# Kernel optimization log

Measured on AMD Instinct MI355X. Metric: run time of the kernel, lower is better.

## Reference

```python
import jax, jax.numpy as jnp
import numpy as np

N = 100_000       # nodes
DEG = 16          # avg degree (fixed here)
E = N * DEG       # edges
IN_F, HID, OUT_F = 64, 32, 16
K, DIM = 3, 2     # n_kernels, pseudo-coordinate dim


def setup_inputs() -> dict:
    key = jax.random.key(0)
    k1, k2, k3, k4, k5, k6, k7 = jax.random.split(key, 7)
    row_ptr = jnp.arange(N + 1, dtype=jnp.int64) * DEG          # CSR offsets, fixed degree
    col_idx = jax.random.randint(k1, (E,), 0, N, dtype=jnp.int64)
    input_feature = jax.random.normal(k2, (N, IN_F), dtype=jnp.float32)
    p = jax.random.uniform(k3, (E, DIM), dtype=jnp.float32)      # pseudo-coordinates per edge
    mu = jax.random.normal(k4, (K, DIM), dtype=jnp.float32)
    sigma = jax.random.uniform(k5, (K, DIM), dtype=jnp.float32, minval=0.5, maxval=1.5)
    W1 = jax.random.normal(k6, (K, IN_F, HID), dtype=jnp.float32) * (1.0 / np.sqrt(IN_F))
    W2 = jax.random.normal(k7, (K, HID, OUT_F), dtype=jnp.float32) * (1.0 / np.sqrt(HID))
    return {"row_ptr": row_ptr, "col_idx": col_idx, "input_feature": input_feature,
            "p": p, "mu": mu, "sigma": sigma, "W1": W1, "W2": W2}


def _edge_gaussians(p, mu, sigma):
    # w[e,k] = exp(-0.5 * sum_d ((p[e,d]-mu[k,d])/sigma[k,d])^2)   [E,K]
    diff = p[:, None, :] - mu[None, :, :]                 # [E,K,D]
    inv_var = 1.0 / (sigma * sigma)                       # [K,D]
    return jnp.exp(-0.5 * jnp.sum(diff * diff * inv_var[None], axis=-1))


def _gmm_conv(row_ptr, col_idx, dst, x, gauss, W):
    # per-kernel linear transform first (dense GEMM), then irregular gather+scatter
    xW = jnp.einsum('nf,kfh->nkh', x, W)                  # [N,K,H]
    msg = jnp.einsum('ek,ekh->eh', gauss, xW[col_idx])    # gather + mix kernels  [E,H]
    n_nodes = row_ptr.shape[0] - 1
    return jax.ops.segment_sum(msg, dst, num_segments=n_nodes)  # scatter-add to dst rows


def reference(row_ptr, col_idx, input_feature, p, mu, sigma, W1, W2):
    n_nodes = row_ptr.shape[0] - 1
    deg = jnp.diff(row_ptr)
    dst = jnp.repeat(jnp.arange(n_nodes), deg, total_repeat_length=col_idx.shape[0])
    gauss = _edge_gaussians(p, mu, sigma)                 # shared by both layers
    h = _gmm_conv(row_ptr, col_idx, dst, input_feature, gauss, W1)
    out = _gmm_conv(row_ptr, col_idx, dst, h, gauss, W2)
    return out
```

## Files before the change

### kernel.cpp

```cpp
#include <hip/hip_runtime.h>
#include <hip/hip_fp16.h>


#define KK 3

using half8  = __attribute__((ext_vector_type(8))) _Float16;
using float4v = __attribute__((ext_vector_type(4))) float;

__global__ void prep_kernel(const float* __restrict__ p, const float* __restrict__ mu,
                            const float* __restrict__ sigma, float2* __restrict__ gaussh,
                            const float* __restrict__ x, __half* __restrict__ xh,
                            int E, int NX8) {
    int i = blockIdx.x * blockDim.x + threadIdx.x;
    if (i < E) {
        float p0 = p[2 * i], p1 = p[2 * i + 1];
        float g[KK];
#pragma unroll
        for (int k = 0; k < KK; ++k) {
            float m0 = mu[2 * k], m1 = mu[2 * k + 1];
            float s0 = sigma[2 * k], s1 = sigma[2 * k + 1];
            float d0 = p0 - m0, d1 = p1 - m1;
            float q = (d0 * d0) / (s0 * s0) + (d1 * d1) / (s1 * s1);
            g[k] = __expf(-0.5f * q);
        }
        union { __half h[4]; float2 v; } o;
        o.h[0] = __float2half(g[0]); o.h[1] = __float2half(g[1]);
        o.h[2] = __float2half(g[2]); o.h[3] = __float2half(0.f);
        gaussh[i] = o.v;
    }
    if (i < NX8) {
        float4 v0 = ((const float4*)x)[2 * i];
        float4 v1 = ((const float4*)x)[2 * i + 1];
        union { __half h[8]; float4 v; } o;
        o.h[0] = __float2half(v0.x); o.h[1] = __float2half(v0.y);
        o.h[2] = __float2half(v0.z); o.h[3] = __float2half(v0.w);
        o.h[4] = __float2half(v1.x); o.h[5] = __float2half(v1.y);
        o.h[6] = __float2half(v1.z); o.h[7] = __float2half(v1.w);
        ((float4*)xh)[i] = o.v;
    }
}

__global__ void pack_w(const float* __restrict__ W1, const float* __restrict__ W2,
                       __half* __restrict__ B1, __half* __restrict__ B2) {
    int t = blockIdx.x * blockDim.x + threadIdx.x;
    if (t < 6144) {
        int j = t & 7, lane = (t >> 3) & 63, grp = t >> 9;
        int ot = grp / 6, kb = grp % 6;
        int kidx = kb * 32 + (lane >> 4) * 8 + j;
        int o = ot * 16 + (lane & 15);
        B1[t] = __float2half(W1[kidx * 32 + o]);
    } else if (t < 6144 + 1536) {
        int t2 = t - 6144;
        int j = t2 & 7, lane = (t2 >> 3) & 63, kb = t2 >> 9;
        int kidx = kb * 32 + (lane >> 4) * 8 + j;
        int o = lane & 15;
        B2[t2] = __float2half(W2[kidx * 16 + o]);
    }
}

__device__ __forceinline__ void unpack8(float4 raw, float* f) {
    union { float4 v; __half2 h2[4]; } u;
    u.v = raw;
#pragma unroll
    for (int q = 0; q < 4; ++q) {
        float2 t = __half22float2(u.h2[q]);
        f[2 * q] = t.x; f[2 * q + 1] = t.y;
    }
}

template <int F>
__global__ __launch_bounds__(256) void gather_s(
    const int* __restrict__ row_ptr, const int* __restrict__ col_idx,
    const float2* __restrict__ gaussh, const __half* __restrict__ xh,
    __half* __restrict__ s, int N) {
    constexpr int TPN = F / 8;
    constexpr int J   = KK * F;

    const int t  = blockIdx.x * 256 + threadIdx.x;
    const int n  = t / TPN;
    const int ch = t % TPN;
    if (n >= N) return;

    float a0[8], a1[8], a2[8];
#pragma unroll
    for (int q = 0; q < 8; ++q) { a0[q] = 0.f; a1[q] = 0.f; a2[q] = 0.f; }

    const float4* x4 = (const float4*)xh;

    int e0 = row_ptr[n], e1 = row_ptr[n + 1];
    int e = e0;
    for (; e + 8 <= e1; e += 8) {
        int cols[8];
        float2 gr[8];
        float4 xr[8];
#pragma unroll
        for (int j = 0; j < 8; ++j) cols[j] = col_idx[e + j];
#pragma unroll
        for (int j = 0; j < 8; ++j) gr[j] = gaussh[e + j];
#pragma unroll
        for (int j = 0; j < 8; ++j) xr[j] = x4[(size_t)cols[j] * TPN + ch];
#pragma unroll
        for (int j = 0; j < 8; ++j) {
            union { float2 v; __half2 h2[2]; } ug; ug.v = gr[j];
            float2 gab = __half22float2(ug.h2[0]);
            float2 gc_ = __half22float2(ug.h2[1]);
            float f[8];
            unpack8(xr[j], f);
#pragma unroll
            for (int q = 0; q < 8; ++q) {
                a0[q] = fmaf(gab.x, f[q], a0[q]);
                a1[q] = fmaf(gab.y, f[q], a1[q]);
                a2[q] = fmaf(gc_.x, f[q], a2[q]);
            }
        }
    }
    for (; e < e1; ++e) {
        int c = col_idx[e];
        union { float2 v; __half2 h2[2]; } ug; ug.v = gaussh[e];
        float2 gab = __half22float2(ug.h2[0]);
        float2 gc_ = __half22float2(ug.h2[1]);
        float f[8];
        unpack8(x4[(size_t)c * TPN + ch], f);
#pragma unroll
        for (int q = 0; q < 8; ++q) {
            a0[q] = fmaf(gab.x, f[q], a0[q]);
            a1[q] = fmaf(gab.y, f[q], a1[q]);
            a2[q] = fmaf(gc_.x, f[q], a2[q]);
        }
    }

    __half* srow = s + (size_t)n * J + ch * 8;
    union { __half h[8]; float4 v; } o;
#pragma unroll
    for (int q = 0; q < 8; ++q) o.h[q] = __float2half(a0[q]);
    *(float4*)(srow + 0 * F) = o.v;
#pragma unroll
    for (int q = 0; q < 8; ++q) o.h[q] = __float2half(a1[q]);
    *(float4*)(srow + 1 * F) = o.v;
#pragma unroll
    for (int q = 0; q < 8; ++q) o.h[q] = __float2half(a2[q]);
    *(float4*)(srow + 2 * F) = o.v;
}

template <int J, int H, bool OUT_HALF>
__global__ __launch_bounds__(256) void gemm_mfma(
    const __half* __restrict__ s, const __half* __restrict__ Bpack,
    void* __restrict__ yout, int N) {
    constexpr int KB = J / 32;
    constexpr int OT = H / 16;

    const int lane = threadIdx.x & 63;
    const int gw   = (blockIdx.x * 256 + threadIdx.x) >> 6;
    const int nt   = gw / OT;
    const int ot   = gw % OT;
    const int n0   = nt * 16;
    if (n0 >= N) return;

    const int quad = lane >> 4;
    const int row  = lane & 15;

    half8 b[KB];
#pragma unroll
    for (int kb = 0; kb < KB; ++kb)
        b[kb] = ((const half8*)Bpack)[(ot * KB + kb) * 64 + lane];

    const half8* arow = (const half8*)(s + (size_t)(n0 + row) * J);

    float4v acc = {0.f, 0.f, 0.f, 0.f};
#pragma unroll
    for (int kb = 0; kb < KB; ++kb)
        acc = __builtin_amdgcn_mfma_f32_16x16x32_f16(arow[kb * 4 + quad], b[kb], acc, 0, 0, 0);

    const int col = row;
    const int r0  = quad * 4;
#pragma unroll
    for (int reg = 0; reg < 4; ++reg) {
        int n = n0 + r0 + reg;
        if constexpr (OUT_HALF)
            ((__half*)yout)[(size_t)n * H + ot * 16 + col] = __float2half(acc[reg]);
        else
            ((float*)yout)[(size_t)n * H + col] = acc[reg];
    }
}

extern "C" void kernel_launch(void* const* d_in, const int* in_sizes, int n_in,
                              void* d_out, int out_size, void* d_ws, size_t ws_size,
                              hipStream_t stream) {
    const int* row_ptr  = (const int*)d_in[0];
    const int* col_idx  = (const int*)d_in[1];
    const float* x      = (const float*)d_in[2];
    const float* p      = (const float*)d_in[3];
    const float* mu     = (const float*)d_in[4];
    const float* sigma  = (const float*)d_in[5];
    const float* W1     = (const float*)d_in[6];
    const float* W2     = (const float*)d_in[7];

    const int N = in_sizes[0] - 1;
    const int E = in_sizes[1];

    __half* B1pack = (__half*)d_ws;
    __half* B2pack = B1pack + 6144;
    float2* gaussh = (float2*)(B2pack + 1536);
    __half* xh     = (__half*)(gaussh + (size_t)E);
    __half* hh     = xh + (size_t)N * 64;
    __half* s1     = hh + (size_t)N * 32;
    __half* s2     = s1 + (size_t)N * 192;
    float*  out    = (float*)d_out;

    const int B = 256;
    const int NX8 = N * 8;
    const int prep_n = (E > NX8 ? E : NX8);

    prep_kernel<<<(prep_n + B - 1) / B, B, 0, stream>>>(p, mu, sigma, gaussh, x, xh, E, NX8);
    pack_w<<<30, B, 0, stream>>>(W1, W2, B1pack, B2pack);

    {
        long long T = (long long)N * 8;
        gather_s<64><<<(int)((T + B - 1) / B), B, 0, stream>>>(row_ptr, col_idx, gaussh, xh, s1, N);
        int waves = ((N + 15) / 16) * 2;
        gemm_mfma<192, 32, true><<<(waves + 3) / 4, B, 0, stream>>>(s1, B1pack, (void*)hh, N);
    }
    {
        long long T = (long long)N * 4;
        gather_s<32><<<(int)((T + B - 1) / B), B, 0, stream>>>(row_ptr, col_idx, gaussh, hh, s2, N);
        int waves = (N + 15) / 16;
        gemm_mfma<96, 16, false><<<(waves + 3) / 4, B, 0, stream>>>(s2, B2pack, (void*)out, N);
    }
}
```

Before: 179.5 us.

## Fuse gather and MFMA GEMM per layer via LDS, recompute Gaussians inline

Each layer's gather-aggregate and its MFMA GEMM now run in one kernel. The aggregated [nodes, 3F] tile is staged in padded shared memory instead of being written to and re-read from the global s1/s2 buffers. Edge Gaussian weights are recomputed from p inside both layers instead of being precomputed into a half buffer. Weight packing is merged into the x conversion kernel, cutting the launch count from six to three. In exchange, each layer reads 8 bytes of fp32 p per edge instead of the 8-byte half gauss record and evaluates three exps per edge per thread, repeated across the channel threads. The kernels also add LDS use and a block barrier.

Result: faster. 156.8 us (-12.6%).

```diff
diff --git a/kernel.cpp b/kernel.cpp
--- a/kernel.cpp
+++ b/kernel.cpp
@@ -4,57 +4,33 @@
 
 #define KK 3
 
-using half8  = __attribute__((ext_vector_type(8))) _Float16;
+using half8   = __attribute__((ext_vector_type(8))) _Float16;
 using float4v = __attribute__((ext_vector_type(4))) float;
 
-__global__ void prep_kernel(const float* __restrict__ p, const float* __restrict__ mu,
-                            const float* __restrict__ sigma, float2* __restrict__ gaussh,
-                            const float* __restrict__ x, __half* __restrict__ xh,
-                            int E, int NX8) {
-    int i = blockIdx.x * blockDim.x + threadIdx.x;
-    if (i < E) {
-        float p0 = p[2 * i], p1 = p[2 * i + 1];
-        float g[KK];
-#pragma unroll
-        for (int k = 0; k < KK; ++k) {
-            float m0 = mu[2 * k], m1 = mu[2 * k + 1];
-            float s0 = sigma[2 * k], s1 = sigma[2 * k + 1];
-            float d0 = p0 - m0, d1 = p1 - m1;
-            float q = (d0 * d0) / (s0 * s0) + (d1 * d1) / (s1 * s1);
-            g[k] = __expf(-0.5f * q);
-        }
-        union { __half h[4]; float2 v; } o;
-        o.h[0] = __float2half(g[0]); o.h[1] = __float2half(g[1]);
-        o.h[2] = __float2half(g[2]); o.h[3] = __float2half(0.f);
-        gaussh[i] = o.v;
-    }
-    if (i < NX8) {
-        float4 v0 = ((const float4*)x)[2 * i];
-        float4 v1 = ((const float4*)x)[2 * i + 1];
+__global__ void setup_kernel(const float* __restrict__ x, __half* __restrict__ xh,
+                             const float* __restrict__ W1, const float* __restrict__ W2,
+                             __half* __restrict__ B1, __half* __restrict__ B2, int NX8) {
+    int t = blockIdx.x * blockDim.x + threadIdx.x;
+    if (t < NX8) {
+        float4 v0 = ((const float4*)x)[2 * t];
+        float4 v1 = ((const float4*)x)[2 * t + 1];
         union { __half h[8]; float4 v; } o;
         o.h[0] = __float2half(v0.x); o.h[1] = __float2half(v0.y);
         o.h[2] = __float2half(v0.z); o.h[3] = __float2half(v0.w);
         o.h[4] = __float2half(v1.x); o.h[5] = __float2half(v1.y);
         o.h[6] = __float2half(v1.z); o.h[7] = __float2half(v1.w);
-        ((float4*)xh)[i] = o.v;
-    }
-}
-
-__global__ void pack_w(const float* __restrict__ W1, const float* __restrict__ W2,
-                       __half* __restrict__ B1, __half* __restrict__ B2) {
-    int t = blockIdx.x * blockDim.x + threadIdx.x;
+        ((float4*)xh)[t] = o.v;
+    }
     if (t < 6144) {
         int j = t & 7, lane = (t >> 3) & 63, grp = t >> 9;
         int ot = grp / 6, kb = grp % 6;
         int kidx = kb * 32 + (lane >> 4) * 8 + j;
-        int o = ot * 16 + (lane & 15);
-        B1[t] = __float2half(W1[kidx * 32 + o]);
+        B1[t] = __float2half(W1[kidx * 32 + ot * 16 + (lane & 15)]);
     } else if (t < 6144 + 1536) {
         int t2 = t - 6144;
         int j = t2 & 7, lane = (t2 >> 3) & 63, kb = t2 >> 9;
         int kidx = kb * 32 + (lane >> 4) * 8 + j;
-        int o = lane & 15;
-        B2[t2] = __float2half(W2[kidx * 16 + o]);
+        B2[t2] = __float2half(W2[kidx * 16 + (lane & 15)]);
     }
 }
 
@@ -68,118 +44,139 @@
     }
 }
 
-template <int F>
-__global__ __launch_bounds__(256) void gather_s(
+template <int F, int H, bool OUT_HALF>
+__global__ __launch_bounds__(256) void fused_layer(
     const int* __restrict__ row_ptr, const int* __restrict__ col_idx,
-    const float2* __restrict__ gaussh, const __half* __restrict__ xh,
-    __half* __restrict__ s, int N) {
-    constexpr int TPN = F / 8;
-    constexpr int J   = KK * F;
-
-    const int t  = blockIdx.x * 256 + threadIdx.x;
-    const int n  = t / TPN;
-    const int ch = t % TPN;
-    if (n >= N) return;
+    const float* __restrict__ p, const float* __restrict__ mu, const float* __restrict__ sigma,
+    const __half* __restrict__ xh, const __half* __restrict__ Bpack,
+    void* __restrict__ yout, int N) {
+    constexpr int TPN    = F / 8;
+    constexpr int NODES  = 256 / TPN;
+    constexpr int J      = KK * F;
+    constexpr int STRIDE = (F == 64) ? 200 : 104;
+    constexpr int KB     = J / 32;
+    constexpr int OT     = H / 16;
+    constexpr int TILES  = NODES / 16;
+
+    __shared__ __align__(16) __half sLh[NODES * STRIDE];
+
+    const int tid = threadIdx.x;
+    const int nl  = tid / TPN;
+    const int ch  = tid % TPN;
+    const int n   = blockIdx.x * NODES + nl;
+
+    float gm0[KK], gm1[KK], iv0[KK], iv1[KK];
+#pragma unroll
+    for (int k = 0; k < KK; ++k) {
+        gm0[k] = mu[2 * k];     gm1[k] = mu[2 * k + 1];
+        float s0 = sigma[2 * k], s1 = sigma[2 * k + 1];
+        iv0[k] = 1.f / (s0 * s0); iv1[k] = 1.f / (s1 * s1);
+    }
 
     float a0[8], a1[8], a2[8];
 #pragma unroll
     for (int q = 0; q < 8; ++q) { a0[q] = 0.f; a1[q] = 0.f; a2[q] = 0.f; }
 
     const float4* x4 = (const float4*)xh;
-
-    int e0 = row_ptr[n], e1 = row_ptr[n + 1];
-    int e = e0;
-    for (; e + 8 <= e1; e += 8) {
-        int cols[8];
-        float2 gr[8];
-        float4 xr[8];
-#pragma unroll
-        for (int j = 0; j < 8; ++j) cols[j] = col_idx[e + j];
-#pragma unroll
-        for (int j = 0; j < 8; ++j) gr[j] = gaussh[e + j];
-#pragma unroll
-        for (int j = 0; j < 8; ++j) xr[j] = x4[(size_t)cols[j] * TPN + ch];
-#pragma unroll
-        for (int j = 0; j < 8; ++j) {
-            union { float2 v; __half2 h2[2]; } ug; ug.v = gr[j];
-            float2 gab = __half22float2(ug.h2[0]);
-            float2 gc_ = __half22float2(ug.h2[1]);
-            float f[8];
-            unpack8(xr[j], f);
-#pragma unroll
-            for (int q = 0; q < 8; ++q) {
-                a0[q] = fmaf(gab.x, f[q], a0[q]);
-                a1[q] = fmaf(gab.y, f[q], a1[q]);
-                a2[q] = fmaf(gc_.x, f[q], a2[q]);
+    const float2* p2 = (const float2*)p;
+
+    if (n < N) {
+        int e0 = row_ptr[n], e1 = row_ptr[n + 1];
+        int e = e0;
+        for (; e + 8 <= e1; e += 8) {
+            int cols[8];
+            float2 pv[8];
+            float4 xr[8];
+#pragma unroll
+            for (int j = 0; j < 8; ++j) cols[j] = col_idx[e + j];
+#pragma unroll
+            for (int j = 0; j < 8; ++j) pv[j] = p2[e + j];
+#pragma unroll
+            for (int j = 0; j < 8; ++j) xr[j] = x4[(size_t)cols[j] * TPN + ch];
+#pragma unroll
+            for (int j = 0; j < 8; ++j) {
+                float d00 = pv[j].x - gm0[0], d01 = pv[j].y - gm1[0];
+                float d10 = pv[j].x - gm0[1], d11 = pv[j].y - gm1[1];
+                float d20 = pv[j].x - gm0[2], d21 = pv[j].y - gm1[2];
+                float g0 = __expf(-0.5f * (d00 * d00 * iv0[0] + d01 * d01 * iv1[0]));
+                float g1 = __expf(-0.5f * (d10 * d10 * iv0[1] + d11 * d11 * iv1[1]));
+                float g2 = __expf(-0.5f * (d20 * d20 * iv0[2] + d21 * d21 * iv1[2]));
+                float f[8];
+                unpack8(xr[j], f);
+#pragma unroll
+                for (int q = 0; q < 8; ++q) {
+                    a0[q] = fmaf(g0, f[q], a0[q]);
+                    a1[q] = fmaf(g1, f[q], a1[q]);
+                    a2[q] = fmaf(g2, f[q], a2[q]);
+                }
             }
         }
-    }
-    for (; e < e1; ++e) {
-        int c = col_idx[e];
-        union { float2 v; __half2 h2[2]; } ug; ug.v = gaussh[e];
-        float2 gab = __half22float2(ug.h2[0]);
-        float2 gc_ = __half22float2(ug.h2[1]);
-        float f[8];
-        unpack8(x4[(size_t)c * TPN + ch], f);
-#pragma unroll
-        for (int q = 0; q < 8; ++q) {
-            a0[q] = fmaf(gab.x, f[q], a0[q]);
-            a1[q] = fmaf(gab.y, f[q], a1[q]);
-            a2[q] = fmaf(gc_.x, f[q], a2[q]);
+        for (; e < e1; ++e) {
+            int c = col_idx[e];
+            float2 pv = p2[e];
+            float d00 = pv.x - gm0[0], d01 = pv.y - gm1[0];
+            float d10 = pv.x - gm0[1], d11 = pv.y - gm1[1];
+            float d20 = pv.x - gm0[2], d21 = pv.y - gm1[2];
+            float g0 = __expf(-0.5f * (d00 * d00 * iv0[0] + d01 * d01 * iv1[0]));
+            float g1 = __expf(-0.5f * (d10 * d10 * iv0[1] + d11 * d11 * iv1[1]));
+            float g2 = __expf(-0.5f * (d20 * d20 * iv0[2] + d21 * d21 * iv1[2]));
+            float f[8];
+            unpack8(x4[(size_t)c * TPN + ch], f);
+#pragma unroll
+            for (int q = 0; q < 8; ++q) {
+                a0[q] = fmaf(g0, f[q], a0[q]);
+                a1[q] = fmaf(g1, f[q], a1[q]);
+                a2[q] = fmaf(g2, f[q], a2[q]);
+            }
         }
     }
 
-    __half* srow = s + (size_t)n * J + ch * 8;
-    union { __half h[8]; float4 v; } o;
-#pragma unroll
-    for (int q = 0; q < 8; ++q) o.h[q] = __float2half(a0[q]);
-    *(float4*)(srow + 0 * F) = o.v;
-#pragma unroll
-    for (int q = 0; q < 8; ++q) o.h[q] = __float2half(a1[q]);
-    *(float4*)(srow + 1 * F) = o.v;
-#pragma unroll
-    for (int q = 0; q < 8; ++q) o.h[q] = __float2half(a2[q]);
-    *(float4*)(srow + 2 * F) = o.v;
-}
-
-template <int J, int H, bool OUT_HALF>
-__global__ __launch_bounds__(256) void gemm_mfma(
-    const __half* __restrict__ s, const __half* __restrict__ Bpack,
-    void* __restrict__ yout, int N) {
-    constexpr int KB = J / 32;
-    constexpr int OT = H / 16;
-
-    const int lane = threadIdx.x & 63;
-    const int gw   = (blockIdx.x * 256 + threadIdx.x) >> 6;
-    const int nt   = gw / OT;
-    const int ot   = gw % OT;
-    const int n0   = nt * 16;
-    if (n0 >= N) return;
-
-    const int quad = lane >> 4;
-    const int row  = lane & 15;
-
-    half8 b[KB];
-#pragma unroll
-    for (int kb = 0; kb < KB; ++kb)
-        b[kb] = ((const half8*)Bpack)[(ot * KB + kb) * 64 + lane];
-
-    const half8* arow = (const half8*)(s + (size_t)(n0 + row) * J);
-
-    float4v acc = {0.f, 0.f, 0.f, 0.f};
-#pragma unroll
-    for (int kb = 0; kb < KB; ++kb)
-        acc = __builtin_amdgcn_mfma_f32_16x16x32_f16(arow[kb * 4 + quad], b[kb], acc, 0, 0, 0);
-
-    const int col = row;
-    const int r0  = quad * 4;
-#pragma unroll
-    for (int reg = 0; reg < 4; ++reg) {
-        int n = n0 + r0 + reg;
-        if constexpr (OUT_HALF)
-            ((__half*)yout)[(size_t)n * H + ot * 16 + col] = __float2half(acc[reg]);
-        else
-            ((float*)yout)[(size_t)n * H + col] = acc[reg];
+    {
+        union { __half h[8]; half8 v; } o;
+#pragma unroll
+        for (int q = 0; q < 8; ++q) o.h[q] = __float2half(a0[q]);
+        *(half8*)(sLh + nl * STRIDE + 0 * F + ch * 8) = o.v;
+#pragma unroll
+        for (int q = 0; q < 8; ++q) o.h[q] = __float2half(a1[q]);
+        *(half8*)(sLh + nl * STRIDE + 1 * F + ch * 8) = o.v;
+#pragma unroll
+        for (int q = 0; q < 8; ++q) o.h[q] = __float2half(a2[q]);
+        *(half8*)(sLh + nl * STRIDE + 2 * F + ch * 8) = o.v;
+    }
+    __syncthreads();
+
+    {
+        const int wv   = tid >> 6;
+        const int lane = tid & 63;
+        const int tile = wv / OT;
+        const int ot   = wv % OT;
+        const int n0   = blockIdx.x * NODES + tile * 16;
+        if (n0 < N) {
+            const int quad = lane >> 4;
+            const int m    = lane & 15;
+
+            half8 b[KB];
+#pragma unroll
+            for (int kb = 0; kb < KB; ++kb)
+                b[kb] = ((const half8*)Bpack)[(ot * KB + kb) * 64 + lane];
+
+            const half8* av = (const half8*)(sLh + (size_t)(tile * 16 + m) * STRIDE);
+            float4v acc = {0.f, 0.f, 0.f, 0.f};
+#pragma unroll
+            for (int kb = 0; kb < KB; ++kb)
+                acc = __builtin_amdgcn_mfma_f32_16x16x32_f16(av[kb * 4 + quad], b[kb], acc, 0, 0, 0);
+
+#pragma unroll
+            for (int reg = 0; reg < 4; ++reg) {
+                int nn = n0 + quad * 4 + reg;
+                if (nn < N) {
+                    if constexpr (OUT_HALF)
+                        ((__half*)yout)[(size_t)nn * H + ot * 16 + m] = __float2half(acc[reg]);
+                    else
+                        ((float*)yout)[(size_t)nn * H + m] = acc[reg];
+                }
+            }
+        }
     }
 }
 
@@ -196,34 +193,21 @@
     const float* W2     = (const float*)d_in[7];
 
     const int N = in_sizes[0] - 1;
-    const int E = in_sizes[1];
 
     __half* B1pack = (__half*)d_ws;
     __half* B2pack = B1pack + 6144;
-    float2* gaussh = (float2*)(B2pack + 1536);
-    __half* xh     = (__half*)(gaussh + (size_t)E);
+    __half* xh     = B2pack + 1536;
     __half* hh     = xh + (size_t)N * 64;
-    __half* s1     = hh + (size_t)N * 32;
-    __half* s2     = s1 + (size_t)N * 192;
     float*  out    = (float*)d_out;
 
     const int B = 256;
     const int NX8 = N * 8;
-    const int prep_n = (E > NX8 ? E : NX8);
-
-    prep_kernel<<<(prep_n + B - 1) / B, B, 0, stream>>>(p, mu, sigma, gaussh, x, xh, E, NX8);
-    pack_w<<<30, B, 0, stream>>>(W1, W2, B1pack, B2pack);
-
-    {
-        long long T = (long long)N * 8;
-        gather_s<64><<<(int)((T + B - 1) / B), B, 0, stream>>>(row_ptr, col_idx, gaussh, xh, s1, N);
-        int waves = ((N + 15) / 16) * 2;
-        gemm_mfma<192, 32, true><<<(waves + 3) / 4, B, 0, stream>>>(s1, B1pack, (void*)hh, N);
-    }
-    {
-        long long T = (long long)N * 4;
-        gather_s<32><<<(int)((T + B - 1) / B), B, 0, stream>>>(row_ptr, col_idx, gaussh, hh, s2, N);
-        int waves = (N + 15) / 16;
-        gemm_mfma<96, 16, false><<<(waves + 3) / 4, B, 0, stream>>>(s2, B2pack, (void*)out, N);
-    }
-}
+    const int setup_n = (NX8 > 7680 ? NX8 : 7680);
+
+    setup_kernel<<<(setup_n + B - 1) / B, B, 0, stream>>>(x, xh, W1, W2, B1pack, B2pack, NX8);
+
+    fused_layer<64, 32, true><<<(N + 31) / 32, B, 0, stream>>>(
+        row_ptr, col_idx, p, mu, sigma, xh, B1pack, (void*)hh, N);
+    fused_layer<32, 16, false><<<(N + 63) / 64, B, 0, stream>>>(
+        row_ptr, col_idx, p, mu, sigma, hh, B2pack, (void*)out, N);
+}
```
